# Kernel optimization log

Measured on AMD Instinct MI355X. Metric: run time of the kernel, lower is better.

## Reference

```python
import jax, jax.numpy as jnp
import numpy as np

D_MODEL = 1024
HEADDIM = 64
EXPAND = 2
D_STATE = 128
D_CONV = 4
NGROUPS = 1
D_INNER = EXPAND * D_MODEL            # 2048
NHEADS = D_INNER // HEADDIM           # 32
CONV_DIM = D_INNER + 2 * NGROUPS * D_STATE
D_IN_PROJ = 2 * D_INNER + 2 * NGROUPS * D_STATE + NHEADS
BATCH = 2
SEQLEN = 1024
EPS = 1e-5


def silu(v):
    return v * jax.nn.sigmoid(v)


def setup_inputs() -> dict:
    key = jax.random.key(0)
    ks = jax.random.split(key, 8)
    s = 0.02
    return {
        "x": jax.random.normal(ks[0], (BATCH, SEQLEN, D_MODEL), jnp.float32),
        "in_proj_w": jax.random.normal(ks[1], (D_IN_PROJ, D_MODEL), jnp.float32) * s,
        "conv_w": jax.random.normal(ks[2], (CONV_DIM, D_CONV), jnp.float32) * 0.2,
        "conv_b": jax.random.normal(ks[3], (CONV_DIM,), jnp.float32) * 0.02,
        "dt_bias": jax.random.normal(ks[4], (NHEADS,), jnp.float32) * 0.1,
        "A_log": jax.random.normal(ks[5], (NHEADS,), jnp.float32) * 0.5,
        "D": jax.random.normal(ks[6], (NHEADS,), jnp.float32) * 0.5,
        "norm_w": jnp.ones((D_INNER,), jnp.float32),
        "out_proj_w": jax.random.normal(ks[7], (D_MODEL, D_INNER), jnp.float32) * s,
    }


def _mamba2(x, in_proj_w, conv_w, conv_b, dt_bias, A_log, D, norm_w, out_proj_w):
    b, l, _ = x.shape
    # input projection -> z | xBC | dt
    zxbcdt = x @ in_proj_w.T                                  # [b,l,d_in_proj]
    z, xBC, dt = jnp.split(zxbcdt, [D_INNER, D_INNER + CONV_DIM], axis=-1)
    dt = jax.nn.softplus(dt + dt_bias)                        # [b,l,nh]
    # causal depthwise conv over time, then SiLU
    rhs = conv_w.T[:, None, :]                                # [d_conv, 1, conv_dim]
    xBC = jax.lax.conv_general_dilated(
        xBC, rhs, window_strides=(1,), padding=[(D_CONV - 1, 0)],
        dimension_numbers=("NWC", "WIO", "NWC"), feature_group_count=CONV_DIM)
    xBC = silu(xBC + conv_b)
    xs, Bm, Cm = jnp.split(xBC, [D_INNER, D_INNER + D_STATE], axis=-1)
    xs = xs.reshape(b, l, NHEADS, HEADDIM)                    # [b,l,h,p]
    A = -jnp.exp(A_log)                                       # [nh], negative
    dA = jnp.exp(dt * A)                                      # [b,l,nh] in (0,1)
    # selective scan: h_t = dA_t * h_{t-1} + dt_t * x_t (outer) B_t; y_t = h_t C_t
    def step(h, inp):
        dA_t, x_t, B_t, dt_t, C_t = inp                       # [b,h],[b,h,p],[b,n],[b,h],[b,n]
        h = h * dA_t[:, :, None, None] + jnp.einsum("bh,bhp,bn->bhpn", dt_t, x_t, B_t)
        y = jnp.einsum("bhpn,bn->bhp", h, C_t)
        return h, y

    h0 = jnp.zeros((b, NHEADS, HEADDIM, D_STATE), x.dtype)
    xs_t = xs.transpose(1, 0, 2, 3)
    _, ys = jax.lax.scan(step, h0, (dA.transpose(1, 0, 2), xs_t,
                                    Bm.transpose(1, 0, 2), dt.transpose(1, 0, 2),
                                    Cm.transpose(1, 0, 2)))
    y = ys.transpose(1, 0, 2, 3) + D[None, None, :, None] * xs  # skip term
    y = y.reshape(b, l, D_INNER)
    # gated RMSNorm (norm_before_gate=False): rmsnorm(y * silu(z)) * w
    y = y * silu(z)
    y = y * jax.lax.rsqrt(jnp.mean(y * y, axis=-1, keepdims=True) + EPS) * norm_w
    return y @ out_proj_w.T


def reference(x, in_proj_w, conv_w, conv_b, dt_bias, A_log, D, norm_w, out_proj_w):
    return x + _mamba2(x, in_proj_w, conv_w, conv_b, dt_bias, A_log, D, norm_w, out_proj_w)
```

## Files before the change

kernel.cpp:

```cpp
#include <hip/hip_runtime.h>
#include <hip/hip_bf16.h>
#include <math.h>

#define NHEADS   32
#define CONV_DIM 2304
#define D_INNER  2048
#define SEQLEN   1024
#define NROWS    2048
#define ZX_STR   4352
#define D_MODEL  1024
#define Q        64
#define NCHUNK   16
#define XT_STR   72

typedef __attribute__((ext_vector_type(8))) short bhalf8;
typedef __attribute__((ext_vector_type(8))) short short8;
typedef __attribute__((ext_vector_type(4))) short short4v;
typedef __attribute__((ext_vector_type(4))) float f32x4;

__device__ __forceinline__ float bf2f(__hip_bfloat16 v){ return __bfloat162float(v); }
__device__ __forceinline__ short f2bs(float f){ __hip_bfloat16 h = __float2bfloat16(f); return *(short*)&h; }
__device__ __forceinline__ float s2f(short s){ __hip_bfloat16 h = *(__hip_bfloat16*)&s; return __bfloat162float(h); }
__device__ __forceinline__ float rdin(const void* p, size_t i, int isf){
    return isf ? ((const float*)p)[i] : __bfloat162float(((const __hip_bfloat16*)p)[i]);
}

__global__ __launch_bounds__(256)
void detect_dtype(const unsigned short* __restrict__ p, int* __restrict__ flag,
                  float* __restrict__ rowsum)
{
    for (int i = threadIdx.x; i < NROWS; i += 256) rowsum[i] = 0.f;
    int cnt = 0;
    for (int i = threadIdx.x; i < 4096; i += 256) {
        unsigned short u = p[2 * i];
        int e = (u >> 7) & 0xFF;
        cnt += (e >= 90 && e <= 141) ? 1 : 0;
    }
#pragma unroll
    for (int m = 1; m < 64; m <<= 1) cnt += __shfl_xor(cnt, m);
    __shared__ int red[4];
    if ((threadIdx.x & 63) == 0) red[threadIdx.x >> 6] = cnt;
    __syncthreads();
    if (threadIdx.x == 0) *flag = ((red[0]+red[1]+red[2]+red[3]) < 2048) ? 1 : 0;
}

#define XN8 262144
#define WN8 561152
#define ON8 262144
__global__ __launch_bounds__(256)
void to_bf16_all(const void* __restrict__ xs, const void* __restrict__ ws,
                 const void* __restrict__ os,
                 __hip_bfloat16* __restrict__ xd, __hip_bfloat16* __restrict__ wd,
                 __hip_bfloat16* __restrict__ od, const int* __restrict__ flagp)
{
    const int isf = *flagp;
    int i = blockIdx.x * 256 + threadIdx.x;
    const void* src; __hip_bfloat16* dst; int j;
    if (i < XN8)            { src = xs; dst = xd; j = i; }
    else if (i < XN8 + WN8) { src = ws; dst = wd; j = i - XN8; }
    else                    { src = os; dst = od; j = i - XN8 - WN8; }
    if (isf) {
        const float4* s = (const float4*)src;
        float4 a = s[2 * j], b = s[2 * j + 1];
        short8 r;
        r[0]=f2bs(a.x); r[1]=f2bs(a.y); r[2]=f2bs(a.z); r[3]=f2bs(a.w);
        r[4]=f2bs(b.x); r[5]=f2bs(b.y); r[6]=f2bs(b.z); r[7]=f2bs(b.w);
        ((short8*)dst)[j] = r;
    } else {
        ((float4*)dst)[j] = ((const float4*)src)[j];
    }
}

template<int MODE, int MT, int NT, int WROWS, int WCOLS>
__global__ __launch_bounds__(256)
void gemm_bt(const __hip_bfloat16* __restrict__ A,
             const __hip_bfloat16* __restrict__ W,
             __hip_bfloat16* __restrict__ Cb,
             const void* __restrict__ xraw,
             void* __restrict__ outv,
             const int* __restrict__ flagp,
             int K, int N)
{
    constexpr int FM = MT / WROWS / 16;
    constexpr int FN = NT / WCOLS / 16;
    constexpr int AI = MT / 32;
    constexpr int BI = NT / 32;
    __shared__ short As[MT * 64];
    __shared__ short Bs[NT * 64];
    const int m0 = blockIdx.y * MT;
    const int n0 = blockIdx.x * NT;
    const int wave = threadIdx.x >> 6;
    const int lane = threadIdx.x & 63;
    const int lr8 = lane >> 3, lc8 = lane & 7;
    const int lr  = lane & 15, lq  = lane >> 4;
    const int wm = (wave / WCOLS) * (MT / WROWS);
    const int wn = (wave % WCOLS) * (NT / WCOLS);
    const int swl = lr & 7;

    f32x4 acc[FM][FN];
#pragma unroll
    for (int i = 0; i < FM; ++i)
#pragma unroll
        for (int j = 0; j < FN; ++j) acc[i][j] = (f32x4){0.f,0.f,0.f,0.f};

    for (int k0 = 0; k0 < K; k0 += 64) {
#pragma unroll
        for (int i = 0; i < AI; ++i) {
            const int rt = (wave * AI + i) * 8;
            const __hip_bfloat16* gp = A + (size_t)(m0 + rt + lr8) * K + k0 + ((lc8 ^ lr8) << 3);
            __builtin_amdgcn_global_load_lds(
                (const __attribute__((address_space(1))) void*)gp,
                (__attribute__((address_space(3))) void*)&As[rt * 64], 16, 0, 0);
        }
#pragma unroll
        for (int i = 0; i < BI; ++i) {
            const int rt = (wave * BI + i) * 8;
            const __hip_bfloat16* gp = W + (size_t)(n0 + rt + lr8) * K + k0 + ((lc8 ^ lr8) << 3);
            __builtin_amdgcn_global_load_lds(
                (const __attribute__((address_space(1))) void*)gp,
                (__attribute__((address_space(3))) void*)&Bs[rt * 64], 16, 0, 0);
        }
        __syncthreads();
#pragma unroll
        for (int kk = 0; kk < 64; kk += 32) {
            const int sw = (((kk >> 3) + lq) ^ swl) << 3;
            bhalf8 af[FM], bfv[FN];
#pragma unroll
            for (int t = 0; t < FM; ++t)
                af[t]  = *(const bhalf8*)&As[(wm + t * 16 + lr) * 64 + sw];
#pragma unroll
            for (int t = 0; t < FN; ++t)
                bfv[t] = *(const bhalf8*)&Bs[(wn + t * 16 + lr) * 64 + sw];
#pragma unroll
            for (int ti = 0; ti < FM; ++ti)
#pragma unroll
                for (int tj = 0; tj < FN; ++tj)
                    acc[ti][tj] = __builtin_amdgcn_mfma_f32_16x16x32_bf16(
                        af[ti], bfv[tj], acc[ti][tj], 0, 0, 0);
        }
        __syncthreads();
    }

    const int isf = (MODE == 1) ? *flagp : 0;
#pragma unroll
    for (int ti = 0; ti < FM; ++ti)
#pragma unroll
        for (int tj = 0; tj < FN; ++tj)
#pragma unroll
            for (int r = 0; r < 4; ++r) {
                int m = m0 + wm + ti * 16 + lq * 4 + r;
                int n = n0 + wn + tj * 16 + lr;
                size_t idx = (size_t)m * N + n;
                float v = acc[ti][tj][r];
                if (MODE == 0) {
                    Cb[idx] = __float2bfloat16(v);
                } else {
                    v += rdin(xraw, idx, isf);
                    if (isf) ((float*)outv)[idx] = v;
                    else     ((__hip_bfloat16*)outv)[idx] = __float2bfloat16(v);
                }
            }
}

__global__ __launch_bounds__(256)
void convdt(const __hip_bfloat16* __restrict__ zxb,
            const void* __restrict__ conv_w, const void* __restrict__ conv_b,
            const void* __restrict__ xraw, const void* __restrict__ wraw,
            const void* __restrict__ dt_bias,
            const int* __restrict__ flagp,
            __hip_bfloat16* __restrict__ xs_bf,
            __hip_bfloat16* __restrict__ B_bf,
            __hip_bfloat16* __restrict__ C_bf,
            float* __restrict__ dtp)
{
    __shared__ short smem[11 * CONV_DIM];
    const int isf = *flagp;

    if (blockIdx.x < 256) {
        const int r0 = blockIdx.x * 8;
        const int bstart = r0 & ~(SEQLEN - 1);
        for (int idx = threadIdx.x; idx < 11 * (CONV_DIM / 8); idx += 256) {
            int ii = idx / (CONV_DIM / 8);
            int seg = idx % (CONV_DIM / 8);
            int g = r0 - 3 + ii;
            bhalf8 v;
            if (g >= bstart) {
                v = *(const bhalf8*)&zxb[(size_t)g * ZX_STR + 2048 + seg * 8];
            } else {
#pragma unroll
                for (int j = 0; j < 8; ++j) v[j] = 0;
            }
            *(bhalf8*)&smem[ii * CONV_DIM + seg * 8] = v;
        }
        __syncthreads();

#pragma unroll
        for (int sIt = 0; sIt < 2; ++sIt) {
            const int seg = threadIdx.x + sIt * 256;
            if (seg >= CONV_DIM / 8) break;
            const int c0 = seg * 8;
            float w0[8], w1[8], w2[8], w3[8], bias[8];
#pragma unroll
            for (int j = 0; j < 8; ++j) {
                bias[j] = rdin(conv_b, c0 + j, isf);
                w0[j] = rdin(conv_w, (size_t)(c0 + j) * 4 + 0, isf);
                w1[j] = rdin(conv_w, (size_t)(c0 + j) * 4 + 1, isf);
                w2[j] = rdin(conv_w, (size_t)(c0 + j) * 4 + 2, isf);
                w3[j] = rdin(conv_w, (size_t)(c0 + j) * 4 + 3, isf);
            }
#pragma unroll
            for (int r = 0; r < 8; ++r) {
                bhalf8 i0 = *(const bhalf8*)&smem[(r + 0) * CONV_DIM + c0];
                bhalf8 i1 = *(const bhalf8*)&smem[(r + 1) * CONV_DIM + c0];
                bhalf8 i2 = *(const bhalf8*)&smem[(r + 2) * CONV_DIM + c0];
                bhalf8 i3 = *(const bhalf8*)&smem[(r + 3) * CONV_DIM + c0];
                bhalf8 out;
#pragma unroll
                for (int j = 0; j < 8; ++j) {
                    float acc = bias[j];
                    acc = fmaf(s2f(i0[j]), w0[j], acc);
                    acc = fmaf(s2f(i1[j]), w1[j], acc);
                    acc = fmaf(s2f(i2[j]), w2[j], acc);
                    acc = fmaf(s2f(i3[j]), w3[j], acc);
                    out[j] = f2bs(acc / (1.f + expf(-acc)));
                }
                const int row = r0 + r;
                if (c0 < 2048)
                    *(bhalf8*)&xs_bf[(size_t)row * 2048 + c0] = out;
                else if (c0 < 2176)
                    *(bhalf8*)&B_bf[(size_t)row * 128 + (c0 - 2048)] = out;
                else
                    *(bhalf8*)&C_bf[(size_t)row * 128 + (c0 - 2176)] = out;
            }
        }
    } else {
        float* xsh = (float*)smem;
        const int r0 = (blockIdx.x - 256) * 8;
        for (int idx = threadIdx.x; idx < 8 * D_MODEL; idx += 256)
            xsh[idx] = rdin(xraw, (size_t)r0 * D_MODEL + idx, isf);
        __syncthreads();
        const int h = threadIdx.x >> 3;
        const int t = threadIdx.x & 7;
        const size_t wbase = (size_t)(4352 + h) * D_MODEL;
        float s[8];
#pragma unroll
        for (int r = 0; r < 8; ++r) s[r] = 0.f;
        for (int k = t; k < D_MODEL; k += 8) {
            float wv = rdin(wraw, wbase + k, isf);
#pragma unroll
            for (int r = 0; r < 8; ++r) s[r] = fmaf(xsh[r * D_MODEL + k], wv, s[r]);
        }
#pragma unroll
        for (int r = 0; r < 8; ++r) {
            s[r] += __shfl_xor(s[r], 1);
            s[r] += __shfl_xor(s[r], 2);
            s[r] += __shfl_xor(s[r], 4);
        }
        if (t == 0) {
            float bias = rdin(dt_bias, h, isf);
#pragma unroll
            for (int r = 0; r < 8; ++r) {
                float raw = s[r] + bias;
                dtp[(size_t)(r0 + r) * NHEADS + h] = raw > 20.f ? raw : log1pf(expf(raw));
            }
        }
    }
}

__global__ __launch_bounds__(256)
void chunk_kernel(const __hip_bfloat16* __restrict__ xs_bf,
                  const __hip_bfloat16* __restrict__ B_bf,
                  const __hip_bfloat16* __restrict__ C_bf,
                  const float* __restrict__ dtp, const void* __restrict__ Alog,
                  const int* __restrict__ flagp,
                  float* __restrict__ cumg, float* __restrict__ decayg,
                  __hip_bfloat16* __restrict__ M_bf,
                  __hip_bfloat16* __restrict__ Sb)
{
    __shared__ float cumS[Q], uS[Q], dtS[Q];
    __shared__ short Xt[64 * XT_STR];
    __shared__ short Bt[128 * XT_STR];
    const int bhc = blockIdx.x;
    const int c = bhc & 15, h = (bhc >> 4) & 31, b = bhc >> 9;
    const int row0 = b * SEQLEN + c * Q;
    const int isf = *flagp;

    if (threadIdx.x < 64) {
        const int t = threadIdx.x;
        const float An = -expf(rdin(Alog, h, isf));
        const float dt = dtp[(size_t)(row0 + t) * NHEADS + h];
        float cum = dt * An;
#pragma unroll
        for (int ofs = 1; ofs < 64; ofs <<= 1) {
            float v = __shfl_up(cum, ofs);
            if (t >= ofs) cum += v;
        }
        float tot = __shfl(cum, 63);
        cumS[t] = cum; dtS[t] = dt;
        uS[t] = expf(tot - cum) * dt;
        cumg[(size_t)bhc * Q + t] = cum;
        if (t == 63) decayg[bhc] = expf(tot);
    }
    __syncthreads();

#pragma unroll
    for (int i = 0; i < 2; ++i) {
        int seg = threadIdx.x + i * 256;
        int t = seg >> 3, p8 = (seg & 7) * 8;
        float ut = uS[t];
        bhalf8 v = *(const bhalf8*)&xs_bf[(size_t)(row0 + t) * 2048 + h * 64 + p8];
#pragma unroll
        for (int j = 0; j < 8; ++j)
            Xt[(p8 + j) * XT_STR + t] = f2bs(s2f(v[j]) * ut);
    }
#pragma unroll
    for (int i = 0; i < 4; ++i) {
        int seg = threadIdx.x + i * 256;
        int t = seg >> 4, n8 = (seg & 15) * 8;
        bhalf8 v = *(const bhalf8*)&B_bf[(size_t)(row0 + t) * 128 + n8];
#pragma unroll
        for (int j = 0; j < 8; ++j)
            Bt[(n8 + j) * XT_STR + t] = v[j];
    }

    const int wave = threadIdx.x >> 6, lane = threadIdx.x & 63;
    const int lr = lane & 15, lq = lane >> 4;

    {
        const int t0 = wave * 16;
        f32x4 acc[4];
#pragma unroll
        for (int j = 0; j < 4; ++j) acc[j] = (f32x4){0.f,0.f,0.f,0.f};
#pragma unroll
        for (int kk = 0; kk < 128; kk += 32) {
            bhalf8 af = *(const bhalf8*)&C_bf[(size_t)(row0 + t0 + lr) * 128 + kk + lq * 8];
#pragma unroll
            for (int j = 0; j < 4; ++j) {
                bhalf8 bf = *(const bhalf8*)&B_bf[(size_t)(row0 + j * 16 + lr) * 128 + kk + lq * 8];
                acc[j] = __builtin_amdgcn_mfma_f32_16x16x32_bf16(af, bf, acc[j], 0, 0, 0);
            }
        }
#pragma unroll
        for (int j = 0; j < 4; ++j)
#pragma unroll
            for (int r = 0; r < 4; ++r) {
                int t = t0 + lq * 4 + r;
                int s = j * 16 + lr;
                float m = (s <= t) ? acc[j][r] * expf(cumS[t] - cumS[s]) * dtS[s] : 0.f;
                M_bf[(size_t)bhc * 4096 + t * 64 + s] = __float2bfloat16(m);
            }
    }
    __syncthreads();

    {
        const int p0 = wave * 16;
        f32x4 acc[8];
#pragma unroll
        for (int j = 0; j < 8; ++j) acc[j] = (f32x4){0.f,0.f,0.f,0.f};
#pragma unroll
        for (int kk = 0; kk < 64; kk += 32) {
            bhalf8 af = *(const bhalf8*)&Xt[(p0 + lr) * XT_STR + kk + lq * 8];
#pragma unroll
            for (int j = 0; j < 8; ++j) {
                bhalf8 bf = *(const bhalf8*)&Bt[(j * 16 + lr) * XT_STR + kk + lq * 8];
                acc[j] = __builtin_amdgcn_mfma_f32_16x16x32_bf16(af, bf, acc[j], 0, 0, 0);
            }
        }
#pragma unroll
        for (int j = 0; j < 8; ++j)
#pragma unroll
            for (int r = 0; r < 4; ++r) {
                int p = p0 + lq * 4 + r;
                int n = j * 16 + lr;
                Sb[(size_t)bhc * 8192 + p * 128 + n] = __float2bfloat16(acc[j][r]);
            }
    }
}

__global__ __launch_bounds__(256)
void rec_kernel(const __hip_bfloat16* __restrict__ Sb,
                const float* __restrict__ decayg,
                __hip_bfloat16* __restrict__ hst)
{
    const int bh = blockIdx.x >> 3;
    const int sl = blockIdx.x & 7;
    const int off = sl * 1024 + threadIdx.x * 4;
    float h0 = 0.f, h1 = 0.f, h2 = 0.f, h3 = 0.f;
    for (int c = 0; c < NCHUNK; ++c) {
        size_t base = ((size_t)bh * NCHUNK + c) * 8192 + off;
        short4v hb;
        hb[0] = f2bs(h0); hb[1] = f2bs(h1); hb[2] = f2bs(h2); hb[3] = f2bs(h3);
        *(short4v*)&hst[base] = hb;
        short4v sv = *(const short4v*)&Sb[base];
        float d = decayg[bh * NCHUNK + c];
        h0 = fmaf(h0, d, s2f(sv[0])); h1 = fmaf(h1, d, s2f(sv[1]));
        h2 = fmaf(h2, d, s2f(sv[2])); h3 = fmaf(h3, d, s2f(sv[3]));
    }
}

__global__ __launch_bounds__(256)
void y_kernel(const __hip_bfloat16* __restrict__ M_bf,
              const __hip_bfloat16* __restrict__ xs_bf,
              const __hip_bfloat16* __restrict__ C_bf,
              const __hip_bfloat16* __restrict__ hst,
              const float* __restrict__ cumg,
              const __hip_bfloat16* __restrict__ zxb,
              const void* __restrict__ Draw, const int* __restrict__ flagp,
              __hip_bfloat16* __restrict__ vbuf, float* __restrict__ rowsum)
{
    __shared__ short Xt[64 * XT_STR];
    __shared__ short zS[64 * XT_STR];
    const int bhc = blockIdx.x;
    const int c = bhc & 15, h = (bhc >> 4) & 31, b = bhc >> 9;
    const int row0 = b * SEQLEN + c * Q;
    const int isf = *flagp;
    const float Dh = rdin(Draw, h, isf);

#pragma unroll
    for (int i = 0; i < 2; ++i) {
        int seg = threadIdx.x + i * 256;
        int t = seg >> 3, p8 = (seg & 7) * 8;
        bhalf8 v = *(const bhalf8*)&xs_bf[(size_t)(row0 + t) * 2048 + h * 64 + p8];
#pragma unroll
        for (int j = 0; j < 8; ++j)
            Xt[(p8 + j) * XT_STR + t] = v[j];
        bhalf8 zv = *(const bhalf8*)&zxb[(size_t)(row0 + t) * ZX_STR + h * 64 + p8];
        *(bhalf8*)&zS[t * XT_STR + p8] = zv;
    }
    __syncthreads();

    const int wave = threadIdx.x >> 6, lane = threadIdx.x & 63;
    const int lr = lane & 15, lq = lane >> 4;
    const int t0 = wave * 16;
    f32x4 acc1[4], acc2[4];
#pragma unroll
    for (int j = 0; j < 4; ++j) { acc1[j] = (f32x4){0.f,0.f,0.f,0.f}; acc2[j] = acc1[j]; }

#pragma unroll
    for (int kk = 0; kk < 64; kk += 32) {
        bhalf8 af = *(const bhalf8*)&M_bf[(size_t)bhc * 4096 + (t0 + lr) * 64 + kk + lq * 8];
#pragma unroll
        for (int j = 0; j < 4; ++j) {
            bhalf8 bf = *(const bhalf8*)&Xt[(j * 16 + lr) * XT_STR + kk + lq * 8];
            acc1[j] = __builtin_amdgcn_mfma_f32_16x16x32_bf16(af, bf, acc1[j], 0, 0, 0);
        }
    }
#pragma unroll
    for (int kk = 0; kk < 128; kk += 32) {
        bhalf8 af = *(const bhalf8*)&C_bf[(size_t)(row0 + t0 + lr) * 128 + kk + lq * 8];
#pragma unroll
        for (int j = 0; j < 4; ++j) {
            bhalf8 bf = *(const bhalf8*)&hst[(size_t)bhc * 8192 + (j * 16 + lr) * 128 + kk + lq * 8];
            acc2[j] = __builtin_amdgcn_mfma_f32_16x16x32_bf16(af, bf, acc2[j], 0, 0, 0);
        }
    }
    float ex[4];
#pragma unroll
    for (int r = 0; r < 4; ++r) ex[r] = expf(cumg[(size_t)bhc * Q + t0 + lq * 4 + r]);

    float vv[4][4];
    float s2[4] = {0.f, 0.f, 0.f, 0.f};
#pragma unroll
    for (int j = 0; j < 4; ++j)
#pragma unroll
        for (int r = 0; r < 4; ++r) {
            int t = t0 + lq * 4 + r;
            int p = j * 16 + lr;
            float xv = s2f(Xt[p * XT_STR + t]);
            float y = acc1[j][r] + ex[r] * acc2[j][r] + Dh * xv;
            float zz = s2f(zS[t * XT_STR + p]);
            float v = y * (zz / (1.f + expf(-zz)));
            vv[j][r] = v;
            s2[r] += v * v;
        }
#pragma unroll
    for (int r = 0; r < 4; ++r) {
        s2[r] += __shfl_xor(s2[r], 1);
        s2[r] += __shfl_xor(s2[r], 2);
        s2[r] += __shfl_xor(s2[r], 4);
        s2[r] += __shfl_xor(s2[r], 8);
    }
    if (lr == 0)
#pragma unroll
        for (int r = 0; r < 4; ++r)
            atomicAdd(&rowsum[row0 + t0 + lq * 4 + r], s2[r]);

    __syncthreads();
#pragma unroll
    for (int j = 0; j < 4; ++j)
#pragma unroll
        for (int r = 0; r < 4; ++r)
            zS[(t0 + lq * 4 + r) * XT_STR + j * 16 + lr] = f2bs(vv[j][r]);
    __syncthreads();
#pragma unroll
    for (int i = 0; i < 2; ++i) {
        int seg = threadIdx.x + i * 256;
        int t = seg >> 3, p8 = (seg & 7) * 8;
        bhalf8 o = *(const bhalf8*)&zS[t * XT_STR + p8];
        *(bhalf8*)&vbuf[(size_t)(row0 + t) * D_INNER + h * 64 + p8] = o;
    }
}

__global__ __launch_bounds__(256)
void gate_scale(const __hip_bfloat16* __restrict__ vbuf,
                const float* __restrict__ rowsum,
                const void* __restrict__ norm_w,
                const int* __restrict__ flagp,
                __hip_bfloat16* __restrict__ yg)
{
    const int isf = *flagp;
    const int row = blockIdx.x;
    const float scale = rsqrtf(rowsum[row] / (float)D_INNER + 1e-5f);
    const int seg = threadIdx.x;
    bhalf8 v8 = *(const bhalf8*)&vbuf[(size_t)row * D_INNER + seg * 8];
    bhalf8 o;
#pragma unroll
    for (int j = 0; j < 8; ++j)
        o[j] = f2bs(s2f(v8[j]) * scale * rdin(norm_w, seg * 8 + j, isf));
    *(bhalf8*)&yg[(size_t)row * D_INNER + seg * 8] = o;
}

extern "C" void kernel_launch(void* const* d_in, const int* in_sizes, int n_in,
                              void* d_out, int out_size, void* d_ws, size_t ws_size,
                              hipStream_t stream)
{
    const void* x_raw    = d_in[0];
    const void* inw_raw  = d_in[1];
    const void* convw    = d_in[2];
    const void* convb    = d_in[3];
    const void* dtb      = d_in[4];
    const void* Alog     = d_in[5];
    const void* Dsk      = d_in[6];
    const void* normw    = d_in[7];
    const void* outw_raw = d_in[8];

    char* ws = (char*)d_ws;
    size_t off = 0;
    int* flag = (int*)(ws + off);                      off += 256;
    float* rowsum = (float*)(ws + off);                off += (size_t)NROWS * 4;
    __hip_bfloat16* xb    = (__hip_bfloat16*)(ws+off); off += (size_t)NROWS * D_MODEL * 2;
    __hip_bfloat16* inwb  = (__hip_bfloat16*)(ws+off); off += (size_t)4384 * D_MODEL * 2;
    __hip_bfloat16* outwb = (__hip_bfloat16*)(ws+off); off += (size_t)D_MODEL * D_INNER * 2;
    __hip_bfloat16* zxb   = (__hip_bfloat16*)(ws+off); off += (size_t)NROWS * ZX_STR * 2;
    __hip_bfloat16* xs_bf = (__hip_bfloat16*)(ws+off); off += (size_t)NROWS * 2048 * 2;
    __hip_bfloat16* B_bf  = (__hip_bfloat16*)(ws+off); off += (size_t)NROWS * 128 * 2;
    __hip_bfloat16* C_bf  = (__hip_bfloat16*)(ws+off); off += (size_t)NROWS * 128 * 2;
    float* dtp   = (float*)(ws+off);                   off += (size_t)NROWS * NHEADS * 4;
    float* cumg  = (float*)(ws+off);                   off += (size_t)1024 * Q * 4;
    float* decayg= (float*)(ws+off);                   off += (size_t)1024 * 4;
    __hip_bfloat16* M_bf  = (__hip_bfloat16*)(ws+off); off += (size_t)1024 * 4096 * 2;
    __hip_bfloat16* hst   = (__hip_bfloat16*)(ws+off); off += (size_t)1024 * 8192 * 2;
    __hip_bfloat16* Sb    = (__hip_bfloat16*)(ws+off); off += (size_t)1024 * 8192 * 2;
    __hip_bfloat16* vbuf = Sb;
    __hip_bfloat16* yg   = Sb + (size_t)NROWS * D_INNER;

    detect_dtype<<<1, 256, 0, stream>>>((const unsigned short*)x_raw, flag, rowsum);
    to_bf16_all<<<(XN8+WN8+ON8)/256, 256, 0, stream>>>(x_raw, inw_raw, outw_raw,
                                                       xb, inwb, outwb, flag);
    gemm_bt<0,64,128,1,4><<<dim3(34, 32), 256, 0, stream>>>(
        xb, inwb, zxb, nullptr, nullptr, flag, D_MODEL, ZX_STR);
    convdt<<<512, 256, 0, stream>>>(zxb, convw, convb, x_raw, inw_raw, dtb, flag,
                                    xs_bf, B_bf, C_bf, dtp);
    chunk_kernel<<<1024, 256, 0, stream>>>(xs_bf, B_bf, C_bf, dtp, Alog, flag,
                                           cumg, decayg, M_bf, Sb);
    rec_kernel<<<512, 256, 0, stream>>>(Sb, decayg, hst);
    y_kernel<<<1024, 256, 0, stream>>>(M_bf, xs_bf, C_bf, hst, cumg, zxb, Dsk,
                                       flag, vbuf, rowsum);
    gate_scale<<<NROWS, 256, 0, stream>>>(vbuf, rowsum, normw, flag, yg);
    gemm_bt<1,64,64,2,2><<<dim3(16, 32), 256, 0, stream>>>(
        yg, outwb, nullptr, x_raw, d_out, flag, D_INNER, D_MODEL);
}
```

Baseline: 248.8 us.

## Fold RMSNorm into out-proj GEMM and weights, restructure conv/dt kernel

Removes the gate_scale kernel. The norm weight is folded into the bf16 out_proj weights during conversion, and the per-row rsqrt scale is applied in the out-proj GEMM epilogue. This drops one full read and write pass over the 2048x2048 activation buffer. The conv part of convdt now runs one row per thread group across 2304 blocks with direct global loads instead of a shared-memory tile. The dt projection loads are vectorised. The trade-off is that each thread rereads its overlapping input rows and conv weights from global memory.

Measured after the change: 270.8 us. 8.8% more time.

```diff
diff --git a/kernel.cpp b/kernel.cpp
--- a/kernel.cpp
+++ b/kernel.cpp
@@ -49,25 +49,45 @@
 #define ON8 262144
 __global__ __launch_bounds__(256)
 void to_bf16_all(const void* __restrict__ xs, const void* __restrict__ ws,
-                 const void* __restrict__ os,
+                 const void* __restrict__ os, const void* __restrict__ normw,
                  __hip_bfloat16* __restrict__ xd, __hip_bfloat16* __restrict__ wd,
                  __hip_bfloat16* __restrict__ od, const int* __restrict__ flagp)
 {
     const int isf = *flagp;
     int i = blockIdx.x * 256 + threadIdx.x;
-    const void* src; __hip_bfloat16* dst; int j;
-    if (i < XN8)            { src = xs; dst = xd; j = i; }
-    else if (i < XN8 + WN8) { src = ws; dst = wd; j = i - XN8; }
-    else                    { src = os; dst = od; j = i - XN8 - WN8; }
-    if (isf) {
-        const float4* s = (const float4*)src;
-        float4 a = s[2 * j], b = s[2 * j + 1];
+    if (i < XN8 + WN8) {
+        const void* src; __hip_bfloat16* dst; int j;
+        if (i < XN8) { src = xs; dst = xd; j = i; }
+        else         { src = ws; dst = wd; j = i - XN8; }
+        if (isf) {
+            const float4* s = (const float4*)src;
+            float4 a = s[2 * j], b = s[2 * j + 1];
+            short8 r;
+            r[0]=f2bs(a.x); r[1]=f2bs(a.y); r[2]=f2bs(a.z); r[3]=f2bs(a.w);
+            r[4]=f2bs(b.x); r[5]=f2bs(b.y); r[6]=f2bs(b.z); r[7]=f2bs(b.w);
+            ((short8*)dst)[j] = r;
+        } else {
+            ((float4*)dst)[j] = ((const float4*)src)[j];
+        }
+    } else {
+        int j = i - XN8 - WN8;
+        int k0 = (j * 8) & (D_INNER - 1);
+        float v[8];
+        if (isf) {
+            const float4* s = (const float4*)os;
+            float4 a = s[2 * j], b = s[2 * j + 1];
+            v[0]=a.x; v[1]=a.y; v[2]=a.z; v[3]=a.w;
+            v[4]=b.x; v[5]=b.y; v[6]=b.z; v[7]=b.w;
+        } else {
+            bhalf8 a = ((const bhalf8*)os)[j];
+#pragma unroll
+            for (int q = 0; q < 8; ++q) v[q] = s2f(a[q]);
+        }
         short8 r;
-        r[0]=f2bs(a.x); r[1]=f2bs(a.y); r[2]=f2bs(a.z); r[3]=f2bs(a.w);
-        r[4]=f2bs(b.x); r[5]=f2bs(b.y); r[6]=f2bs(b.z); r[7]=f2bs(b.w);
-        ((short8*)dst)[j] = r;
-    } else {
-        ((float4*)dst)[j] = ((const float4*)src)[j];
+#pragma unroll
+        for (int q = 0; q < 8; ++q)
+            r[q] = f2bs(v[q] * rdin(normw, k0 + q, isf));
+        ((short8*)od)[j] = r;
     }
 }
 
@@ -78,6 +98,7 @@
              __hip_bfloat16* __restrict__ Cb,
              const void* __restrict__ xraw,
              void* __restrict__ outv,
+             const float* __restrict__ rowsum,
              const int* __restrict__ flagp,
              int K, int N)
 {
@@ -155,7 +176,8 @@
                 if (MODE == 0) {
                     Cb[idx] = __float2bfloat16(v);
                 } else {
-                    v += rdin(xraw, idx, isf);
+                    float scale = rsqrtf(rowsum[m] / (float)D_INNER + 1e-5f);
+                    v = v * scale + rdin(xraw, idx, isf);
                     if (isf) ((float*)outv)[idx] = v;
                     else     ((__hip_bfloat16*)outv)[idx] = __float2bfloat16(v);
                 }
@@ -173,82 +195,86 @@
             __hip_bfloat16* __restrict__ C_bf,
             float* __restrict__ dtp)
 {
-    __shared__ short smem[11 * CONV_DIM];
+    __shared__ float xsh[8 * D_MODEL];
     const int isf = *flagp;
 
-    if (blockIdx.x < 256) {
-        const int r0 = blockIdx.x * 8;
-        const int bstart = r0 & ~(SEQLEN - 1);
-        for (int idx = threadIdx.x; idx < 11 * (CONV_DIM / 8); idx += 256) {
-            int ii = idx / (CONV_DIM / 8);
-            int seg = idx % (CONV_DIM / 8);
-            int g = r0 - 3 + ii;
-            bhalf8 v;
+    if (blockIdx.x < 2304) {
+        const int bx = blockIdx.x % 9, by = blockIdx.x / 9;
+        const int seg = bx * 32 + (threadIdx.x & 31);
+        const int c0 = seg * 8;
+        const int row = by * 8 + (threadIdx.x >> 5);
+        const int bstart = row & ~(SEQLEN - 1);
+        bhalf8 in[4];
+#pragma unroll
+        for (int j = 0; j < 4; ++j) {
+            int g = row - 3 + j;
             if (g >= bstart) {
-                v = *(const bhalf8*)&zxb[(size_t)g * ZX_STR + 2048 + seg * 8];
+                in[j] = *(const bhalf8*)&zxb[(size_t)g * ZX_STR + 2048 + c0];
             } else {
 #pragma unroll
-                for (int j = 0; j < 8; ++j) v[j] = 0;
-            }
-            *(bhalf8*)&smem[ii * CONV_DIM + seg * 8] = v;
-        }
-        __syncthreads();
-
-#pragma unroll
-        for (int sIt = 0; sIt < 2; ++sIt) {
-            const int seg = threadIdx.x + sIt * 256;
-            if (seg >= CONV_DIM / 8) break;
-            const int c0 = seg * 8;
-            float w0[8], w1[8], w2[8], w3[8], bias[8];
-#pragma unroll
-            for (int j = 0; j < 8; ++j) {
-                bias[j] = rdin(conv_b, c0 + j, isf);
-                w0[j] = rdin(conv_w, (size_t)(c0 + j) * 4 + 0, isf);
-                w1[j] = rdin(conv_w, (size_t)(c0 + j) * 4 + 1, isf);
-                w2[j] = rdin(conv_w, (size_t)(c0 + j) * 4 + 2, isf);
-                w3[j] = rdin(conv_w, (size_t)(c0 + j) * 4 + 3, isf);
-            }
-#pragma unroll
-            for (int r = 0; r < 8; ++r) {
-                bhalf8 i0 = *(const bhalf8*)&smem[(r + 0) * CONV_DIM + c0];
-                bhalf8 i1 = *(const bhalf8*)&smem[(r + 1) * CONV_DIM + c0];
-                bhalf8 i2 = *(const bhalf8*)&smem[(r + 2) * CONV_DIM + c0];
-                bhalf8 i3 = *(const bhalf8*)&smem[(r + 3) * CONV_DIM + c0];
-                bhalf8 out;
-#pragma unroll
-                for (int j = 0; j < 8; ++j) {
-                    float acc = bias[j];
-                    acc = fmaf(s2f(i0[j]), w0[j], acc);
-                    acc = fmaf(s2f(i1[j]), w1[j], acc);
-                    acc = fmaf(s2f(i2[j]), w2[j], acc);
-                    acc = fmaf(s2f(i3[j]), w3[j], acc);
-                    out[j] = f2bs(acc / (1.f + expf(-acc)));
-                }
-                const int row = r0 + r;
-                if (c0 < 2048)
-                    *(bhalf8*)&xs_bf[(size_t)row * 2048 + c0] = out;
-                else if (c0 < 2176)
-                    *(bhalf8*)&B_bf[(size_t)row * 128 + (c0 - 2048)] = out;
-                else
-                    *(bhalf8*)&C_bf[(size_t)row * 128 + (c0 - 2176)] = out;
-            }
-        }
+                for (int q = 0; q < 8; ++q) in[j][q] = 0;
+            }
+        }
+        bhalf8 out;
+#pragma unroll
+        for (int j = 0; j < 8; ++j) {
+            const int c = c0 + j;
+            float acc = rdin(conv_b, c, isf);
+            acc = fmaf(s2f(in[0][j]), rdin(conv_w, (size_t)c * 4 + 0, isf), acc);
+            acc = fmaf(s2f(in[1][j]), rdin(conv_w, (size_t)c * 4 + 1, isf), acc);
+            acc = fmaf(s2f(in[2][j]), rdin(conv_w, (size_t)c * 4 + 2, isf), acc);
+            acc = fmaf(s2f(in[3][j]), rdin(conv_w, (size_t)c * 4 + 3, isf), acc);
+            out[j] = f2bs(acc / (1.f + expf(-acc)));
+        }
+        if (c0 < 2048)      *(bhalf8*)&xs_bf[(size_t)row * 2048 + c0] = out;
+        else if (c0 < 2176) *(bhalf8*)&B_bf[(size_t)row * 128 + (c0 - 2048)] = out;
+        else                *(bhalf8*)&C_bf[(size_t)row * 128 + (c0 - 2176)] = out;
     } else {
-        float* xsh = (float*)smem;
-        const int r0 = (blockIdx.x - 256) * 8;
-        for (int idx = threadIdx.x; idx < 8 * D_MODEL; idx += 256)
-            xsh[idx] = rdin(xraw, (size_t)r0 * D_MODEL + idx, isf);
+        const int r0 = (blockIdx.x - 2304) * 8;
+        if (isf) {
+            const float4* xp = (const float4*)xraw;
+            for (int i4 = threadIdx.x; i4 < 2048; i4 += 256)
+                *(float4*)&xsh[i4 * 4] = xp[(size_t)r0 * 256 + i4];
+        } else {
+            const bhalf8* xp = (const bhalf8*)xraw;
+            for (int i8 = threadIdx.x; i8 < 1024; i8 += 256) {
+                bhalf8 v = xp[(size_t)r0 * 128 + i8];
+#pragma unroll
+                for (int q = 0; q < 8; ++q) xsh[i8 * 8 + q] = s2f(v[q]);
+            }
+        }
         __syncthreads();
         const int h = threadIdx.x >> 3;
         const int t = threadIdx.x & 7;
-        const size_t wbase = (size_t)(4352 + h) * D_MODEL;
+        const size_t wb = (size_t)(4352 + h) * D_MODEL;
         float s[8];
 #pragma unroll
         for (int r = 0; r < 8; ++r) s[r] = 0.f;
-        for (int k = t; k < D_MODEL; k += 8) {
-            float wv = rdin(wraw, wbase + k, isf);
-#pragma unroll
-            for (int r = 0; r < 8; ++r) s[r] = fmaf(xsh[r * D_MODEL + k], wv, s[r]);
+        if (isf) {
+            const float4* wp = (const float4*)wraw;
+            for (int k0 = 0; k0 < D_MODEL; k0 += 32) {
+                float4 w4 = wp[(wb + k0) / 4 + t];
+#pragma unroll
+                for (int r = 0; r < 8; ++r) {
+                    float4 x4 = *(const float4*)&xsh[r * D_MODEL + k0 + t * 4];
+                    s[r] = fmaf(w4.x, x4.x, fmaf(w4.y, x4.y,
+                           fmaf(w4.z, x4.z, fmaf(w4.w, x4.w, s[r]))));
+                }
+            }
+        } else {
+            const __hip_bfloat16* wp = (const __hip_bfloat16*)wraw;
+            for (int k0 = 0; k0 < D_MODEL; k0 += 64) {
+                bhalf8 w8 = *(const bhalf8*)&wp[wb + k0 + t * 8];
+#pragma unroll
+                for (int r = 0; r < 8; ++r) {
+                    float4 xa = *(const float4*)&xsh[r * D_MODEL + k0 + t * 8];
+                    float4 xb = *(const float4*)&xsh[r * D_MODEL + k0 + t * 8 + 4];
+                    s[r] = fmaf(s2f(w8[0]), xa.x, fmaf(s2f(w8[1]), xa.y,
+                           fmaf(s2f(w8[2]), xa.z, fmaf(s2f(w8[3]), xa.w, s[r]))));
+                    s[r] = fmaf(s2f(w8[4]), xb.x, fmaf(s2f(w8[5]), xb.y,
+                           fmaf(s2f(w8[6]), xb.z, fmaf(s2f(w8[7]), xb.w, s[r]))));
+                }
+            }
         }
 #pragma unroll
         for (int r = 0; r < 8; ++r) {
@@ -499,25 +525,6 @@
         bhalf8 o = *(const bhalf8*)&zS[t * XT_STR + p8];
         *(bhalf8*)&vbuf[(size_t)(row0 + t) * D_INNER + h * 64 + p8] = o;
     }
-}
-
-__global__ __launch_bounds__(256)
-void gate_scale(const __hip_bfloat16* __restrict__ vbuf,
-                const float* __restrict__ rowsum,
-                const void* __restrict__ norm_w,
-                const int* __restrict__ flagp,
-                __hip_bfloat16* __restrict__ yg)
-{
-    const int isf = *flagp;
-    const int row = blockIdx.x;
-    const float scale = rsqrtf(rowsum[row] / (float)D_INNER + 1e-5f);
-    const int seg = threadIdx.x;
-    bhalf8 v8 = *(const bhalf8*)&vbuf[(size_t)row * D_INNER + seg * 8];
-    bhalf8 o;
-#pragma unroll
-    for (int j = 0; j < 8; ++j)
-        o[j] = f2bs(s2f(v8[j]) * scale * rdin(norm_w, seg * 8 + j, isf));
-    *(bhalf8*)&yg[(size_t)row * D_INNER + seg * 8] = o;
 }
 
 extern "C" void kernel_launch(void* const* d_in, const int* in_sizes, int n_in,
@@ -552,21 +559,19 @@
     __hip_bfloat16* hst   = (__hip_bfloat16*)(ws+off); off += (size_t)1024 * 8192 * 2;
     __hip_bfloat16* Sb    = (__hip_bfloat16*)(ws+off); off += (size_t)1024 * 8192 * 2;
     __hip_bfloat16* vbuf = Sb;
-    __hip_bfloat16* yg   = Sb + (size_t)NROWS * D_INNER;
 
     detect_dtype<<<1, 256, 0, stream>>>((const unsigned short*)x_raw, flag, rowsum);
     to_bf16_all<<<(XN8+WN8+ON8)/256, 256, 0, stream>>>(x_raw, inw_raw, outw_raw,
-                                                       xb, inwb, outwb, flag);
+                                                       normw, xb, inwb, outwb, flag);
     gemm_bt<0,64,128,1,4><<<dim3(34, 32), 256, 0, stream>>>(
-        xb, inwb, zxb, nullptr, nullptr, flag, D_MODEL, ZX_STR);
-    convdt<<<512, 256, 0, stream>>>(zxb, convw, convb, x_raw, inw_raw, dtb, flag,
-                                    xs_bf, B_bf, C_bf, dtp);
+        xb, inwb, zxb, nullptr, nullptr, nullptr, flag, D_MODEL, ZX_STR);
+    convdt<<<2560, 256, 0, stream>>>(zxb, convw, convb, x_raw, inw_raw, dtb, flag,
+                                     xs_bf, B_bf, C_bf, dtp);
     chunk_kernel<<<1024, 256, 0, stream>>>(xs_bf, B_bf, C_bf, dtp, Alog, flag,
                                            cumg, decayg, M_bf, Sb);
     rec_kernel<<<512, 256, 0, stream>>>(Sb, decayg, hst);
     y_kernel<<<1024, 256, 0, stream>>>(M_bf, xs_bf, C_bf, hst, cumg, zxb, Dsk,
                                        flag, vbuf, rowsum);
-    gate_scale<<<NROWS, 256, 0, stream>>>(vbuf, rowsum, normw, flag, yg);
     gemm_bt<1,64,64,2,2><<<dim3(16, 32), 256, 0, stream>>>(
-        yg, outwb, nullptr, x_raw, d_out, flag, D_INNER, D_MODEL);
-}
+        vbuf, outwb, nullptr, x_raw, d_out, rowsum, flag, D_INNER, D_MODEL);
+}
```
